# Kernel optimization log

Hardware: AMD Instinct MI355X
Metric: run time of the kernel (lower is better)

Reference implementation:

```python
import jax, jax.numpy as jnp
import numpy as np

RESOLUTION = (128, 128, 128, 150)
FEATURE_DIM = 16
MULTIRES = (1, 2)
# plane (i, j) -> torch tensor (1, F, res[i], res[j]); grid_sample x-coord = coords[..., i] maps to W (res[j]),
# grid_sample y-coord = coords[..., j] maps to H (res[i]).
PAIRS = ((0, 1), (0, 2), (1, 2), (0, 3), (1, 3), (2, 3))


def _xavier_plane(key, f, h, w):
    fan_in = f * h * w
    fan_out = 1 * h * w
    bound = np.sqrt(6.0 / (fan_in + fan_out))
    return jax.random.uniform(key, (f, h, w), jnp.float32, -bound, bound)


def _bilinear_border(plane, gx, gy):
    """F.grid_sample(mode='bilinear', padding_mode='border', align_corners=True).
    plane: (F, H, W); gx, gy: (P,) in [-1, 1]. Returns (P, F)."""
    Fc, H, W = plane.shape
    ix = jnp.clip((gx + 1.0) * 0.5 * (W - 1), 0.0, W - 1)
    iy = jnp.clip((gy + 1.0) * 0.5 * (H - 1), 0.0, H - 1)
    x0 = jnp.floor(ix)
    y0 = jnp.floor(iy)
    x0i = x0.astype(jnp.int32)
    y0i = y0.astype(jnp.int32)
    x1i = jnp.minimum(x0i + 1, W - 1)
    y1i = jnp.minimum(y0i + 1, H - 1)
    wx = ix - x0
    wy = iy - y0
    v00 = plane[:, y0i, x0i]  # (F, P)
    v01 = plane[:, y0i, x1i]
    v10 = plane[:, y1i, x0i]
    v11 = plane[:, y1i, x1i]
    out = (v00 * (1.0 - wx) + v01 * wx) * (1.0 - wy) + (v10 * (1.0 - wx) + v11 * wx) * wy
    return out.T  # (P, F)


def _hexplane_forward(coords, planes):
    # coords: (B, N, 4); planes: flat list of 6*len(MULTIRES) arrays (F, H, W)
    B, N, _ = coords.shape
    c = coords.reshape(-1, 4)  # (P, 4)
    feats = []
    k = 0
    for _level in MULTIRES:
        for (i, j) in PAIRS:
            feats.append(_bilinear_border(planes[k], c[:, i], c[:, j]))
            k += 1
    out = jnp.concatenate(feats, axis=-1)  # (P, 6*F*len(MULTIRES))
    return out.reshape(B, N, -1)


def setup_inputs() -> dict:
    key = jax.random.key(0)
    kc, kp = jax.random.split(key)
    B, N = 2, 400000
    coords = jax.random.uniform(kc, (B, N, 4), jnp.float32, -1.0, 1.0)
    inp = {"coords": coords}
    idx = 0
    for li, level in enumerate(MULTIRES):
        res = [r // level for r in RESOLUTION]
        for pi, (i, j) in enumerate(PAIRS):
            kp, sub = jax.random.split(kp)
            inp[f"p{li}{pi}"] = _xavier_plane(sub, FEATURE_DIM, res[i], res[j])
            idx += 1
    return inp


def reference(coords, p00, p01, p02, p03, p04, p05, p10, p11, p12, p13, p14, p15):
    planes = [p00, p01, p02, p03, p04, p05, p10, p11, p12, p13, p14, p15]
    return _hexplane_forward(coords, planes)
```

## Files before the change

### kernel.cpp

```cpp
#include <hip/hip_runtime.h>

#define FDIM 16

struct PlanePtrs { const float* p[12]; };

__device__ __forceinline__ void plane_dims(int k, int& H, int& W, int& toff,
                                           int& isel, int& jsel) {
    int pi  = (k >= 6) ? (k - 6) : k;
    int lvl = (k >= 6) ? 1 : 0;
    isel = (2320 >> (2 * pi)) & 3;
    jsel = (4073 >> (2 * pi)) & 3;
    H = ((isel == 3) ? 150 : 128) >> lvl;
    W = ((jsel == 3) ? 150 : 128) >> lvl;
    if (k < 6) {
        toff = (k < 3) ? k * 16384 : 49152 + (k - 3) * 19200;
    } else {
        int kk = k - 6;
        toff = 106752 + ((kk < 3) ? kk * 4096 : 12288 + (kk - 3) * 4800);
    }
}

__global__ void __launch_bounds__(256) hex_transpose(PlanePtrs ptrs,
                                                     float4* __restrict__ ws4) {
    int k = blockIdx.y;
    int H, W, toff, isel, jsel;
    plane_dims(k, H, W, toff, isel, jsel);
    int HW = H * W;
    int t = blockIdx.x * 256 + threadIdx.x;
    if (t >= HW) return;
    const float* __restrict__ src = ptrs.p[k];
    float v[FDIM];
#pragma unroll
    for (int f = 0; f < FDIM; ++f) v[f] = src[f * HW + t];
    float4* dst = ws4 + (size_t)(toff + t) * 4;
#pragma unroll
    for (int j = 0; j < 4; ++j)
        dst[j] = make_float4(v[4 * j], v[4 * j + 1], v[4 * j + 2], v[4 * j + 3]);
}

__global__ void __launch_bounds__(256) hex_sample(const float4* __restrict__ coords,
                                                  const float4* __restrict__ ws4,
                                                  float4* __restrict__ out4,
                                                  int total) {
    int idx = blockIdx.x * 256 + threadIdx.x;
    if (idx >= total) return;
    int q = idx & 3;
    int r = idx >> 2;
    int k = r % 12;
    int p = r / 12;

    float4 c = coords[p];

    int H, W, toff, isel, jsel;
    plane_dims(k, H, W, toff, isel, jsel);

    float gx = (isel == 0) ? c.x : (isel == 1) ? c.y : c.z;
    float gy = (jsel == 1) ? c.y : (jsel == 2) ? c.z : c.w;

    float fx = (gx + 1.0f) * 0.5f * (float)(W - 1);
    fx = fminf(fmaxf(fx, 0.0f), (float)(W - 1));
    float fy = (gy + 1.0f) * 0.5f * (float)(H - 1);
    fy = fminf(fmaxf(fy, 0.0f), (float)(H - 1));

    float x0f = floorf(fx), y0f = floorf(fy);
    int x0 = (int)x0f, y0 = (int)y0f;
    int x1 = min(x0 + 1, W - 1);
    int y1 = min(y0 + 1, H - 1);
    float wx = fx - x0f, wy = fy - y0f;

    const float4* base = ws4 + (size_t)toff * 4 + q;
    float4 v00 = base[(y0 * W + x0) * 4];
    float4 v01 = base[(y0 * W + x1) * 4];
    float4 v10 = base[(y1 * W + x0) * 4];
    float4 v11 = base[(y1 * W + x1) * 4];

    float w00 = (1.0f - wx) * (1.0f - wy);
    float w01 = wx * (1.0f - wy);
    float w10 = (1.0f - wx) * wy;
    float w11 = wx * wy;

    float4 o;
    o.x = v00.x * w00 + v01.x * w01 + v10.x * w10 + v11.x * w11;
    o.y = v00.y * w00 + v01.y * w01 + v10.y * w10 + v11.y * w11;
    o.z = v00.z * w00 + v01.z * w01 + v10.z * w10 + v11.z * w11;
    o.w = v00.w * w00 + v01.w * w01 + v10.w * w10 + v11.w * w11;

    out4[idx] = o;
}

extern "C" void kernel_launch(void* const* d_in, const int* in_sizes, int n_in,
                              void* d_out, int out_size, void* d_ws, size_t ws_size,
                              hipStream_t stream) {
    const float4* coords = (const float4*)d_in[0];
    PlanePtrs pp;
    for (int i = 0; i < 12; ++i) pp.p[i] = (const float*)d_in[1 + i];
    float4* ws4  = (float4*)d_ws;
    float4* out4 = (float4*)d_out;

    int points = in_sizes[0] / 4;

    dim3 tgrid(75, 12);
    hex_transpose<<<tgrid, 256, 0, stream>>>(pp, ws4);

    int total  = points * 48;
    int blocks = (total + 255) / 256;
    hex_sample<<<blocks, 256, 0, stream>>>(coords, ws4, out4, total);
}
```

Baseline: 832.3 us.

## Map one thread per point-plane with plane on grid y, nontemporal stores

Reassigns work so each thread handles one point for one plane (plane index from blockIdx.y) and loops over all 16 features, instead of one thread per 4-feature chunk. This removes the per-thread div/mod indexing, makes each block's gathers come from a single plane for better cache locality, and rewrites the blend as lerps. Output is written with nontemporal stores to avoid polluting cache. In exchange, output writes are strided by 192 bytes across threads, giving less coalesced stores, and each thread keeps more loads in flight.

```diff
diff --git a/kernel.cpp b/kernel.cpp
--- a/kernel.cpp
+++ b/kernel.cpp
@@ -1,6 +1,8 @@
 #include <hip/hip_runtime.h>
 
 #define FDIM 16
+
+typedef float f32x4 __attribute__((ext_vector_type(4)));
 
 struct PlanePtrs { const float* p[12]; };
 
@@ -40,19 +42,16 @@
 
 __global__ void __launch_bounds__(256) hex_sample(const float4* __restrict__ coords,
                                                   const float4* __restrict__ ws4,
-                                                  float4* __restrict__ out4,
-                                                  int total) {
-    int idx = blockIdx.x * 256 + threadIdx.x;
-    if (idx >= total) return;
-    int q = idx & 3;
-    int r = idx >> 2;
-    int k = r % 12;
-    int p = r / 12;
-
-    float4 c = coords[p];
+                                                  f32x4* __restrict__ out4,
+                                                  int points) {
+    int p = blockIdx.x * 256 + threadIdx.x;
+    if (p >= points) return;
+    int k = blockIdx.y;
 
     int H, W, toff, isel, jsel;
     plane_dims(k, H, W, toff, isel, jsel);
+
+    float4 c = coords[p];
 
     float gx = (isel == 0) ? c.x : (isel == 1) ? c.y : c.z;
     float gy = (jsel == 1) ? c.y : (jsel == 2) ? c.z : c.w;
@@ -68,24 +67,36 @@
     int y1 = min(y0 + 1, H - 1);
     float wx = fx - x0f, wy = fy - y0f;
 
-    const float4* base = ws4 + (size_t)toff * 4 + q;
-    float4 v00 = base[(y0 * W + x0) * 4];
-    float4 v01 = base[(y0 * W + x1) * 4];
-    float4 v10 = base[(y1 * W + x0) * 4];
-    float4 v11 = base[(y1 * W + x1) * 4];
+    const float4* __restrict__ base = ws4 + (size_t)toff * 4;
+    int i00 = (y0 * W + x0) * 4;
+    int i01 = (y0 * W + x1) * 4;
+    int i10 = (y1 * W + x0) * 4;
+    int i11 = (y1 * W + x1) * 4;
 
-    float w00 = (1.0f - wx) * (1.0f - wy);
-    float w01 = wx * (1.0f - wy);
-    float w10 = (1.0f - wx) * wy;
-    float w11 = wx * wy;
+    f32x4* o = out4 + ((size_t)p * 12 + k) * 4;
 
-    float4 o;
-    o.x = v00.x * w00 + v01.x * w01 + v10.x * w10 + v11.x * w11;
-    o.y = v00.y * w00 + v01.y * w01 + v10.y * w10 + v11.y * w11;
-    o.z = v00.z * w00 + v01.z * w01 + v10.z * w10 + v11.z * w11;
-    o.w = v00.w * w00 + v01.w * w01 + v10.w * w10 + v11.w * w11;
-
-    out4[idx] = o;
+#pragma unroll
+    for (int q = 0; q < 4; ++q) {
+        float4 v00 = base[i00 + q];
+        float4 v01 = base[i01 + q];
+        float4 v10 = base[i10 + q];
+        float4 v11 = base[i11 + q];
+        float4 t0, t1;
+        t0.x = v00.x + (v01.x - v00.x) * wx;
+        t0.y = v00.y + (v01.y - v00.y) * wx;
+        t0.z = v00.z + (v01.z - v00.z) * wx;
+        t0.w = v00.w + (v01.w - v00.w) * wx;
+        t1.x = v10.x + (v11.x - v10.x) * wx;
+        t1.y = v10.y + (v11.y - v10.y) * wx;
+        t1.z = v10.z + (v11.z - v10.z) * wx;
+        t1.w = v10.w + (v11.w - v10.w) * wx;
+        f32x4 r;
+        r.x = t0.x + (t1.x - t0.x) * wy;
+        r.y = t0.y + (t1.y - t0.y) * wy;
+        r.z = t0.z + (t1.z - t0.z) * wy;
+        r.w = t0.w + (t1.w - t0.w) * wy;
+        __builtin_nontemporal_store(r, o + q);
+    }
 }
 
 extern "C" void kernel_launch(void* const* d_in, const int* in_sizes, int n_in,
@@ -95,14 +106,13 @@
     PlanePtrs pp;
     for (int i = 0; i < 12; ++i) pp.p[i] = (const float*)d_in[1 + i];
     float4* ws4  = (float4*)d_ws;
-    float4* out4 = (float4*)d_out;
+    f32x4* out4  = (f32x4*)d_out;
 
     int points = in_sizes[0] / 4;
 
     dim3 tgrid(75, 12);
     hex_transpose<<<tgrid, 256, 0, stream>>>(pp, ws4);
 
-    int total  = points * 48;
-    int blocks = (total + 255) / 256;
-    hex_sample<<<blocks, 256, 0, stream>>>(coords, ws4, out4, total);
+    dim3 sgrid((points + 255) / 256, 12);
+    hex_sample<<<sgrid, 256, 0, stream>>>(coords, ws4, out4, points);
 }
```

New measurement: 2.180 ms. 162% more time.
